# Performance work log

Measured on AMD Instinct MI355X. Metric: run time of the kernel, lower is better.

## Reference

```python
import math
import jax, jax.numpy as jnp
import numpy as np

K_TOP = 8
D_HEAD = 32


def causal_topk_adjacency(x, K):
    # Binary adjacency: for each position t, top-K strictly-causal (j < t)
    # neighbours by dot-product similarity. Rows with < K valid positions
    # (e.g. t=0 has none) get only their valid entries (possibly zero rows).
    B, T, D = x.shape
    sim = jnp.einsum('btd,bsd->bts', x, x) / math.sqrt(D)  # (B,T,T)
    causal = jnp.tril(jnp.ones((T, T), dtype=bool), k=-1)   # j < t
    neg = jnp.finfo(sim.dtype).min
    sim_m = jnp.where(causal[None], sim, neg)
    vals, idx = jax.lax.top_k(sim_m, K)                      # (B,T,K)
    valid = (vals > neg).astype(x.dtype)
    b = jnp.arange(B)[:, None, None]
    t = jnp.arange(T)[None, :, None]
    A = jnp.zeros((B, T, T), x.dtype).at[b, t, idx].max(valid)
    return A


def setup_inputs() -> dict:
    key = jax.random.key(0)
    ks = jax.random.split(key, 3)
    B, T, D = 2, 4096, 1024
    x = jax.random.normal(ks[0], (B, T, D), dtype=jnp.float32)
    W_q = jax.random.normal(ks[1], (D_HEAD, D), dtype=jnp.float32) * (1.0 / math.sqrt(D))
    W_k = jax.random.normal(ks[2], (D_HEAD, D), dtype=jnp.float32) * (1.0 / math.sqrt(D))
    gain = jnp.ones((D,), dtype=jnp.float32)
    bias = jnp.zeros((D,), dtype=jnp.float32)
    log_mix = jnp.zeros((), dtype=jnp.float32)
    log_scale = jnp.zeros((), dtype=jnp.float32)
    return {"x": x, "W_q": W_q, "W_k": W_k, "gain": gain, "bias": bias,
            "log_mix": log_mix, "log_scale": log_scale}


def reference(x, W_q, W_k, gain, bias, log_mix, log_scale):
    B, T, D = x.shape
    mix = jax.nn.sigmoid(log_mix)
    scale = jax.nn.softplus(log_scale) + 0.01

    A = causal_topk_adjacency(x, K_TOP)                      # (B,T,T) binary

    q = jnp.einsum('btd,hd->bth', x, W_q)                    # (B,T,Dh)
    k = jnp.einsum('bsd,hd->bsh', x, W_k)
    score = jnp.einsum('bth,bsh->bts', q, k) / math.sqrt(D_HEAD)
    score = jnp.where(A < 0.5, -1e9, score)

    row_max = jax.lax.stop_gradient(jnp.max(score, axis=-1, keepdims=True))
    score = score - row_max
    attn = jax.nn.softmax(score, axis=-1)
    attn = jnp.nan_to_num(attn, nan=0.0)

    msg = jnp.einsum('bts,bsd->btd', attn, x)
    blended = mix * x + (1.0 - mix) * msg
    delta = jax.nn.gelu(blended * gain + bias, approximate=False) * scale
    return delta
```

## Files before the change

kernel.cpp:

```cpp
#include <hip/hip_runtime.h>
#include <math.h>

#define B 2
#define T 4096
#define D 1024
#define DH 32
#define TNB 32
#define NBLK 528
#define NK 12
#define CPR (32*NK)

typedef __bf16 bf16x8 __attribute__((ext_vector_type(8)));
typedef float f32x4 __attribute__((ext_vector_type(4)));
typedef unsigned u32x4 __attribute__((ext_vector_type(4)));

#define AS1 __attribute__((address_space(1)))
#define AS3 __attribute__((address_space(3)))

__device__ __forceinline__ unsigned mono32(float v) {
    unsigned u = __float_as_uint(v);
    u ^= ((unsigned)((int)u >> 31)) | 0x80000000u;
    return u;
}

__device__ __forceinline__ unsigned dpp_umax_bcast(unsigned v) {
    #define DPPMAX(CTRL) { unsigned t_ = (unsigned)__builtin_amdgcn_update_dpp(0, (int)v, CTRL, 0xF, 0xF, true); v = v > t_ ? v : t_; }
    DPPMAX(0x111) DPPMAX(0x112) DPPMAX(0x114) DPPMAX(0x118)
    DPPMAX(0x142) DPPMAX(0x143)
    #undef DPPMAX
    return (unsigned)__builtin_amdgcn_readlane((int)v, 63);
}
__device__ __forceinline__ float dpp_fsum_bcast(float v) {
    #define DPPADD(CTRL) { int t_ = __builtin_amdgcn_update_dpp(0, __float_as_int(v), CTRL, 0xF, 0xF, true); v += __int_as_float(t_); }
    DPPADD(0x111) DPPADD(0x112) DPPADD(0x114) DPPADD(0x118)
    DPPADD(0x142) DPPADD(0x143)
    #undef DPPADD
    return __int_as_float(__builtin_amdgcn_readlane(__float_as_int(v), 63));
}
__device__ __forceinline__ float dpp_gsum8(float p) {
    { int t_ = __builtin_amdgcn_update_dpp(0, __float_as_int(p), 0x0B1, 0xF, 0xF, true); p += __int_as_float(t_); }
    { int t_ = __builtin_amdgcn_update_dpp(0, __float_as_int(p), 0x04E, 0xF, 0xF, true); p += __int_as_float(t_); }
    { int t_ = __builtin_amdgcn_update_dpp(0, __float_as_int(p), 0x141, 0xF, 0xF, true); p += __int_as_float(t_); }
    return p;
}

__device__ __forceinline__ void merge12(const unsigned* a12, const unsigned* b12,
                                        unsigned* o12) {
    unsigned m16[16];
    #pragma unroll
    for (int i = 0; i < 16; ++i) {
        unsigned aa = (i < NK) ? a12[i] : 0u;
        unsigned bb = (15 - i < NK) ? b12[15 - i] : 0u;
        m16[i] = aa > bb ? aa : bb;
    }
    #pragma unroll
    for (int g = 8; g >= 1; g >>= 1) {
        #pragma unroll
        for (int i = 0; i < 16; ++i) {
            if (!(i & g)) {
                unsigned x0 = m16[i], x1 = m16[i + g];
                m16[i]     = x0 > x1 ? x0 : x1;
                m16[i + g] = x0 > x1 ? x1 : x0;
            }
        }
    }
    #pragma unroll
    for (int i = 0; i < NK; ++i) o12[i] = m16[i];
}

__global__ __launch_bounds__(256) void conv_kernel(const float* __restrict__ x,
        __bf16* __restrict__ xhi, __bf16* __restrict__ xlo)
{
    int i = (blockIdx.x * 256 + threadIdx.x) << 3;
    float4 a = *(const float4*)(x + i);
    float4 c = *(const float4*)(x + i + 4);
    float av[8] = {a.x, a.y, a.z, a.w, c.x, c.y, c.z, c.w};
    __bf16 h[8], l[8];
    #pragma unroll
    for (int j = 0; j < 8; ++j) {
        h[j] = (__bf16)av[j];
        l[j] = (__bf16)(av[j] - (float)h[j]);
    }
    *(float4*)(xhi + i) = *(float4*)h;
    *(float4*)(xlo + i) = *(float4*)l;
}

__global__ void mean_kernel(const float* __restrict__ x, float* __restrict__ meansum)
{
    int gid  = blockIdx.x;
    int b    = gid >> 6;
    int rem  = gid & 63;
    int dblk = rem >> 4;
    int tch  = rem & 15;
    int d = dblk * 256 + threadIdx.x;
    const float* xp = x + (b * T + tch * 256) * D + d;
    float s = 0.f;
    #pragma unroll 8
    for (int it = 0; it < 256; ++it) s += xp[it * D];
    atomicAdd(&meansum[(b << 10) + d], s);
}

__global__ __launch_bounds__(256) void qk_mfma_kernel(
        const __bf16* __restrict__ xhi, const __bf16* __restrict__ xlo,
        const __bf16* __restrict__ Whi, const __bf16* __restrict__ Wlo,
        float* __restrict__ qo, float* __restrict__ ko)
{
    __shared__ __align__(16) __bf16 stg[10240];
    __bf16* sAhi = stg;
    __bf16* sAlo = stg + 2560;
    __bf16* sBhi = stg + 5120;
    __bf16* sBlo = stg + 7680;

    int tid = threadIdx.x;
    int m0 = blockIdx.x << 6;
    int w = tid >> 6, lane = tid & 63;
    int fr = lane & 15, fq = lane >> 4;

    int arow = tid >> 2, aq = tid & 3;
    const __bf16* gAh = xhi + (size_t)(m0 + arow) * D + aq * 8;
    const __bf16* gAl = xlo + (size_t)(m0 + arow) * D + aq * 8;
    const __bf16* gBh = Whi + arow * D + aq * 8;
    const __bf16* gBl = Wlo + arow * D + aq * 8;

    f32x4 acc[4];
    #pragma unroll
    for (int j = 0; j < 4; ++j) acc[j] = (f32x4){0.f, 0.f, 0.f, 0.f};

    float4 a0 = *(const float4*)(gAh);
    float4 a1 = *(const float4*)(gAl);
    float4 b0 = *(const float4*)(gBh);
    float4 b1 = *(const float4*)(gBl);

    int sa = arow * 40 + aq * 8;

    for (int kc = 0; kc < 32; ++kc) {
        __syncthreads();
        *(float4*)(sAhi + sa) = a0;
        *(float4*)(sAlo + sa) = a1;
        *(float4*)(sBhi + sa) = b0;
        *(float4*)(sBlo + sa) = b1;
        __syncthreads();
        if (kc + 1 < 32) {
            int k0 = (kc + 1) << 5;
            a0 = *(const float4*)(gAh + k0);
            a1 = *(const float4*)(gAl + k0);
            b0 = *(const float4*)(gBh + k0);
            b1 = *(const float4*)(gBl + k0);
        }
        int r = (w << 4) + fr;
        bf16x8 fah = *(const bf16x8*)(sAhi + r * 40 + fq * 8);
        bf16x8 fal = *(const bf16x8*)(sAlo + r * 40 + fq * 8);
        bf16x8 fbh[4], fbl[4];
        #pragma unroll
        for (int j = 0; j < 4; ++j) {
            int rb = j * 16 + fr;
            fbh[j] = *(const bf16x8*)(sBhi + rb * 40 + fq * 8);
            fbl[j] = *(const bf16x8*)(sBlo + rb * 40 + fq * 8);
        }
        #pragma unroll
        for (int j = 0; j < 4; ++j) {
            acc[j] = __builtin_amdgcn_mfma_f32_16x16x32_bf16(fah, fbh[j], acc[j], 0, 0, 0);
            acc[j] = __builtin_amdgcn_mfma_f32_16x16x32_bf16(fah, fbl[j], acc[j], 0, 0, 0);
            acc[j] = __builtin_amdgcn_mfma_f32_16x16x32_bf16(fal, fbh[j], acc[j], 0, 0, 0);
        }
    }
    int grow0 = m0 + (w << 4) + (fq << 2);
    #pragma unroll
    for (int j = 0; j < 4; ++j) {
        int gn = j * 16 + fr;
        float* dst = (gn < 32) ? (qo + grow0 * DH + gn)
                               : (ko + grow0 * DH + gn - 32);
        dst[0]      = acc[j][0];
        dst[DH]     = acc[j][1];
        dst[2 * DH] = acc[j][2];
        dst[3 * DH] = acc[j][3];
    }
}

__global__ __launch_bounds__(256, 4) void topk_mfma_kernel(
        const __bf16* __restrict__ xhi, unsigned* __restrict__ pkey)
{
    __shared__ __align__(16) char smem[40960];
    __bf16* stg = (__bf16*)smem;
    float* Sbuf = (float*)smem;

    int tid = threadIdx.x;
    int b = blockIdx.x / NBLK;
    int l = blockIdx.x - b * NBLK;
    int rt = (int)((sqrtf(8.f * l + 1.f) - 1.f) * 0.5f);
    while ((rt + 1) * (rt + 2) / 2 <= l) ++rt;
    while (rt * (rt + 1) / 2 > l) --rt;
    int ct = l - rt * (rt + 1) / 2;
    int r0 = rt << 7, c0 = ct << 7;
    int base = b * T;

    int w = tid >> 6, lane = tid & 63;
    int wr = (w >> 1) << 6, wc = (w & 1) << 6;
    bool active = !(rt == ct && w == 1);
    int fr = lane & 15, fq = lane >> 4;
    int fqs = (fq ^ ((fr >> 1) & 3)) << 3;

    int lrow = lane >> 2;
    int lcq = (((lane & 3) ^ ((lane >> 3) & 3)) << 3);
    const __bf16* gA = xhi + (size_t)(base + r0) * D;
    const __bf16* gB = xhi + (size_t)(base + c0) * D;
    const __bf16* gA0 = gA + (size_t)((w << 4) + lrow) * D + lcq;
    const __bf16* gA1 = gA0 + (size_t)64 * D;
    const __bf16* gB0 = gB + (size_t)((w << 4) + lrow) * D + lcq;
    const __bf16* gB1 = gB0 + (size_t)64 * D;

    f32x4 acc[4][4];
    #pragma unroll
    for (int i = 0; i < 4; ++i)
        #pragma unroll
        for (int j = 0; j < 4; ++j) acc[i][j] = (f32x4){0.f, 0.f, 0.f, 0.f};

#define ISSUE_A(BUFBASE, KO) do { \
    __bf16* bA_ = (BUFBASE); \
    __builtin_amdgcn_global_load_lds((const AS1 unsigned int*)(gA0 + (KO)), \
        (AS3 unsigned int*)(bA_ + (w << 9)), 16, 0, 0); \
    __builtin_amdgcn_global_load_lds((const AS1 unsigned int*)(gA1 + (KO)), \
        (AS3 unsigned int*)(bA_ + 2048 + (w << 9)), 16, 0, 0); \
} while (0)
#define ISSUE_B(BUFBASE, KO) do { \
    __bf16* bB_ = (BUFBASE); \
    __builtin_amdgcn_global_load_lds((const AS1 unsigned int*)(gB0 + (KO)), \
        (AS3 unsigned int*)(bB_ + (w << 9)), 16, 0, 0); \
    __builtin_amdgcn_global_load_lds((const AS1 unsigned int*)(gB1 + (KO)), \
        (AS3 unsigned int*)(bB_ + 2048 + (w << 9)), 16, 0, 0); \
} while (0)

    ISSUE_B(stg + 12288, 0);
    ISSUE_A(stg, 0);
    ISSUE_A(stg + 4096, 32);

    int asel = 0, isel = 2;
    for (int kc = 0; kc < 32; ++kc) {
        if (kc < 31) { asm volatile("s_waitcnt vmcnt(2)" ::: "memory"); }
        else         { asm volatile("s_waitcnt vmcnt(0)" ::: "memory"); }
        __builtin_amdgcn_s_barrier();
        asm volatile("" ::: "memory");
        if (kc + 1 < 32)
            ISSUE_B(stg + 12288 + (((kc + 1) & 1) << 12), (kc + 1) << 5);
        if (kc + 2 < 32) {
            ISSUE_A(stg + (isel << 12), (kc + 2) << 5);
            isel = (isel == 2) ? 0 : isel + 1;
        }
        if (active) {
            const __bf16* cA = stg + (asel << 12);
            const __bf16* cB = stg + 12288 + ((kc & 1) << 12);
            bf16x8 ah[4], bh[4];
            #pragma unroll
            for (int i = 0; i < 4; ++i) {
                int ar = wr + i * 16 + fr;
                ah[i] = *(const bf16x8*)(cA + ar * 32 + fqs);
                int bc = wc + i * 16 + fr;
                bh[i] = *(const bf16x8*)(cB + bc * 32 + fqs);
            }
            #pragma unroll
            for (int i = 0; i < 4; ++i)
                #pragma unroll
                for (int j = 0; j < 4; ++j)
                    acc[i][j] = __builtin_amdgcn_mfma_f32_16x16x32_bf16(ah[i], bh[j], acc[i][j], 0, 0, 0);
        }
        asel = (asel == 2) ? 0 : asel + 1;
    }
#undef ISSUE_A
#undef ISSUE_B

    int cr = fq << 2, cc = fr;
    int q = lane >> 4;
    #pragma unroll
    for (int phase = 0; phase < 2; ++phase) {
        __syncthreads();
        if ((w >> 1) == phase) {
            #pragma unroll
            for (int i = 0; i < 4; ++i)
                #pragma unroll
                for (int j = 0; j < 4; ++j) {
                    float* sp = Sbuf + (i * 16 + cr) * 129 + wc + j * 16 + cc;
                    sp[0]       = acc[i][j][0];
                    sp[129]     = acc[i][j][1];
                    sp[2 * 129] = acc[i][j][2];
                    sp[3 * 129] = acc[i][j][3];
                }
        }
        __syncthreads();
        {
            int sr = (w << 4) + (lane & 15);
            int gt = r0 + (phase << 6) + sr;
            int cmax = gt - c0;
            if (cmax > 128) cmax = 128;
            if (cmax < 0) cmax = 0;
            int h0 = q << 5;
            int hmax = cmax < (h0 + 32) ? cmax : (h0 + 32);
            unsigned key[NK];
            #pragma unroll
            for (int i = 0; i < NK; ++i) key[i] = 0u;
            const float* Srow = Sbuf + sr * 129;
            #pragma unroll
            for (int mb = 0; mb < 4; ++mb) {
                int cb = h0 + (((mb + q) & 3) << 3);
                float v[8];
                #pragma unroll
                for (int j = 0; j < 8; ++j) v[j] = Srow[cb + j];
                #pragma unroll
                for (int j = 0; j < 8; ++j) {
                    int c = cb + j;
                    unsigned u = mono32(v[j]);
                    unsigned tk = (c < hmax) ? ((u & 0xFFFFFF80u) | (unsigned)(127 - c)) : 0u;
                    #pragma unroll
                    for (int i = 0; i < NK; ++i) {
                        unsigned hi = key[i] > tk ? key[i] : tk;
                        unsigned lo = key[i] > tk ? tk : key[i];
                        key[i] = hi; tk = lo;
                    }
                }
            }
            #pragma unroll
            for (int lvl = 0; lvl < 2; ++lvl) {
                int xm = 16 << lvl;
                unsigned o12[NK], m12[NK];
                #pragma unroll
                for (int i = 0; i < NK; ++i) o12[i] = __shfl_xor(key[i], xm);
                merge12(key, o12, m12);
                #pragma unroll
                for (int i = 0; i < NK; ++i) key[i] = m12[i];
            }
            if (q < 3) {
                u32x4 ov;
                #pragma unroll
                for (int j = 0; j < 4; ++j) {
                    unsigned k0 = (q == 0) ? key[j] : (q == 1) ? key[4 + j] : key[8 + j];
                    ov[j] = k0 ? ((k0 & 0xFFFFF000u) | ((k0 & 127u) + (unsigned)(3968 - c0))) : 0u;
                }
                *(u32x4*)(pkey + (size_t)(base + gt) * CPR + ct * NK + (q << 2)) = ov;
            }
        }
    }
}

__global__ __launch_bounds__(256) void select_msg_kernel(const float* __restrict__ x,
        const float* __restrict__ q, const float* __restrict__ k,
        const float* __restrict__ meansum,
        const unsigned* __restrict__ pkey,
        const float* __restrict__ gain, const float* __restrict__ bias,
        const float* __restrict__ plm, const float* __restrict__ pls,
        float* __restrict__ out)
{
    int tid = threadIdx.x;
    int w = tid >> 6, lane = tid & 63;
    int rid = (blockIdx.x << 2) + w;
    int b = rid >> 12, t = rid & (T - 1);
    int ncand = NK * ((t + 127) >> 7);

    unsigned cv[6];
    #pragma unroll
    for (int u = 0; u < 6; ++u) {
        int cid = lane + (u << 6);
        cv[u] = (cid < ncand) ? pkey[(size_t)rid * CPR + cid] : 0u;
    }
    const float* xt = x + (size_t)rid * D;
    float4 xt4[4];
    #pragma unroll
    for (int c = 0; c < 4; ++c)
        xt4[c] = *(const float4*)(xt + (c << 8) + (lane << 2));

    unsigned skey[NK]; int sgid[NK];
    #pragma unroll
    for (int i = 0; i < NK; ++i) {
        unsigned m = cv[0];
        #pragma unroll
        for (int u = 1; u < 6; ++u) m = m > cv[u] ? m : cv[u];
        m = dpp_umax_bcast(m);
        skey[i] = m;
        sgid[i] = 4095 - (int)(m & 4095u);
        #pragma unroll
        for (int u = 0; u < 6; ++u) cv[u] = (cv[u] == m) ? 0u : cv[u];
    }

    float ex[NK];
    #pragma unroll
    for (int batch = 0; batch < 3; ++batch) {
        float4 rv[4][4];
        #pragma unroll
        for (int s = 0; s < 4; ++s) {
            int i = batch * 4 + s;
            int row = (skey[i] != 0u) ? sgid[i] : 0;
            const float* xj = x + (size_t)((b << 12) + row) * D;
            #pragma unroll
            for (int c = 0; c < 4; ++c)
                rv[s][c] = *(const float4*)(xj + (c << 8) + (lane << 2));
        }
        #pragma unroll
        for (int s = 0; s < 4; ++s) {
            float ss = 0.f;
            #pragma unroll
            for (int c = 0; c < 4; ++c)
                ss += xt4[c].x * rv[s][c].x + xt4[c].y * rv[s][c].y
                    + xt4[c].z * rv[s][c].z + xt4[c].w * rv[s][c].w;
            ex[batch * 4 + s] = dpp_fsum_bcast(ss);
        }
    }

    unsigned long long top8[8];
    #pragma unroll
    for (int r = 0; r < 8; ++r) top8[r] = 0ull;
    #pragma unroll
    for (int i = 0; i < NK; ++i) {
        unsigned u = mono32(ex[i]);
        unsigned long long t64 = (skey[i] != 0u)
            ? ((((unsigned long long)u) << 12) | (unsigned long long)(4095 - sgid[i]))
            : 0ull;
        #pragma unroll
        for (int r = 0; r < 8; ++r) {
            unsigned long long hi = (t64 > top8[r]) ? t64 : top8[r];
            unsigned long long lo = (t64 > top8[r]) ? top8[r] : t64;
            top8[r] = hi; t64 = lo;
        }
    }
    bool vld[8]; int bidx[8];
    #pragma unroll
    for (int i = 0; i < 8; ++i) {
        vld[i]  = top8[i] != 0ull;
        bidx[i] = 4095 - (int)(top8[i] & 4095ull);
    }

    int i8 = lane >> 3, e = lane & 7;
    unsigned long long kk = (i8 & 4)
        ? ((i8 & 2) ? ((i8 & 1) ? top8[7] : top8[6]) : ((i8 & 1) ? top8[5] : top8[4]))
        : ((i8 & 2) ? ((i8 & 1) ? top8[3] : top8[2]) : ((i8 & 1) ? top8[1] : top8[0]));
    bool v8 = kk != 0ull;
    int g8 = v8 ? (4095 - (int)(kk & 4095ull)) : 0;
    float4 qv = *(const float4*)(q + (size_t)rid * DH + (e << 2));
    float4 kv = *(const float4*)(k + (size_t)((b << 12) + g8) * DH + (e << 2));
    float p = qv.x * kv.x + qv.y * kv.y + qv.z * kv.z + qv.w * kv.w;
    p = dpp_gsum8(p);
    p *= 0.17677669529663687f;

    float sc[8];
    #pragma unroll
    for (int i = 0; i < 8; ++i)
        sc[i] = __int_as_float(__builtin_amdgcn_readlane(__float_as_int(p), i << 3));

    float m = -INFINITY; int cnt = 0;
    #pragma unroll
    for (int i = 0; i < 8; ++i)
        if (vld[i]) { ++cnt; if (sc[i] > m) m = sc[i]; }

    float wgt[8]; float Z = 0.f; int gsel[8];
    #pragma unroll
    for (int i = 0; i < 8; ++i) {
        wgt[i] = vld[i] ? expf(sc[i] - m) : 0.f;
        Z += wgt[i];
        gsel[i] = vld[i] ? ((b << 12) + bidx[i]) : (b << 12);
    }
    float invZ = (cnt > 0) ? 1.f / Z : 0.f;
    #pragma unroll
    for (int i = 0; i < 8; ++i) wgt[i] *= invZ;

    float mix   = 1.f / (1.f + expf(-plm[0]));
    float scale = log1pf(expf(pls[0])) + 0.01f;
    const float onemix = 1.f - mix;

    float4 msg4[4];
    if (cnt == 0) {
        #pragma unroll
        for (int c = 0; c < 4; ++c) {
            float4 ms = *(const float4*)(meansum + (b << 10) + (c << 8) + (lane << 2));
            msg4[c].x = ms.x * (1.f / (float)T); msg4[c].y = ms.y * (1.f / (float)T);
            msg4[c].z = ms.z * (1.f / (float)T); msg4[c].w = ms.w * (1.f / (float)T);
        }
    } else {
        #pragma unroll
        for (int c = 0; c < 4; ++c) msg4[c] = (float4){0.f, 0.f, 0.f, 0.f};
        #pragma unroll
        for (int g = 0; g < 2; ++g) {
            float4 rv[4][4];
            #pragma unroll
            for (int s = 0; s < 4; ++s) {
                const float* xj = x + (size_t)gsel[g * 4 + s] * D;
                #pragma unroll
                for (int c = 0; c < 4; ++c)
                    rv[s][c] = *(const float4*)(xj + (c << 8) + (lane << 2));
            }
            #pragma unroll
            for (int s = 0; s < 4; ++s) {
                float wi = wgt[g * 4 + s];
                #pragma unroll
                for (int c = 0; c < 4; ++c) {
                    msg4[c].x += wi * rv[s][c].x; msg4[c].y += wi * rv[s][c].y;
                    msg4[c].z += wi * rv[s][c].z; msg4[c].w += wi * rv[s][c].w;
                }
            }
        }
    }
    #pragma unroll
    for (int c = 0; c < 4; ++c) {
        int d0 = (c << 8) + (lane << 2);
        float4 g4 = *(const float4*)(gain + d0);
        float4 b4 = *(const float4*)(bias + d0);
        float4 xv = xt4[c];
        float zi[4] = {
            (mix * xv.x + onemix * msg4[c].x) * g4.x + b4.x,
            (mix * xv.y + onemix * msg4[c].y) * g4.y + b4.y,
            (mix * xv.z + onemix * msg4[c].z) * g4.z + b4.z,
            (mix * xv.w + onemix * msg4[c].w) * g4.w + b4.w };
        float4 o4;
        o4.x = 0.5f * zi[0] * (1.f + erff(zi[0] * 0.70710678118654752f)) * scale;
        o4.y = 0.5f * zi[1] * (1.f + erff(zi[1] * 0.70710678118654752f)) * scale;
        o4.z = 0.5f * zi[2] * (1.f + erff(zi[2] * 0.70710678118654752f)) * scale;
        o4.w = 0.5f * zi[3] * (1.f + erff(zi[3] * 0.70710678118654752f)) * scale;
        *(float4*)(out + (size_t)rid * D + d0) = o4;
    }
}

extern "C" void kernel_launch(void* const* d_in, const int* in_sizes, int n_in,
                              void* d_out, int out_size, void* d_ws, size_t ws_size,
                              hipStream_t stream)
{
    const float* x    = (const float*)d_in[0];
    const float* Wq   = (const float*)d_in[1];
    const float* Wk   = (const float*)d_in[2];
    const float* gain = (const float*)d_in[3];
    const float* bias = (const float*)d_in[4];
    const float* plm  = (const float*)d_in[5];
    const float* pls  = (const float*)d_in[6];
    float* out = (float*)d_out;

    float* ws      = (float*)d_ws;
    float* q       = ws;
    float* k       = ws + 262144;
    float* meansum = ws + 524288;
    unsigned* pkey = (unsigned*)(ws + 526336);
    __bf16* xhi    = (__bf16*)(ws + 3672064);
    __bf16* xlo    = xhi + (size_t)B * T * D;
    __bf16* Whi    = xlo + (size_t)B * T * D;
    __bf16* Wlo    = Whi + 64 * D;

    hipMemsetAsync(meansum, 0, 2048 * sizeof(float), stream);
    conv_kernel<<<B * T * D / 2048, 256, 0, stream>>>(x, xhi, xlo);
    conv_kernel<<<16, 256, 0, stream>>>(Wq, Whi, Wlo);
    conv_kernel<<<16, 256, 0, stream>>>(Wk, Whi + 32 * D, Wlo + 32 * D);
    mean_kernel<<<128, 256, 0, stream>>>(x, meansum);
    qk_mfma_kernel<<<B * T / 64, 256, 0, stream>>>(xhi, xlo, Whi, Wlo, q, k);
    topk_mfma_kernel<<<B * NBLK, 256, 0, stream>>>(xhi, pkey);
    select_msg_kernel<<<B * T / 4, 256, 0, stream>>>(x, q, k, meansum, pkey,
                                                     gain, bias, plm, pls, out);
}
```

Before: 262.6 us.

## Fuse prep kernels and merge QK projection with top-k launch

The x and W bf16 conversion kernels and the column-mean kernel become one prep launch. The mean now writes per-chunk partial sums, so the memset and atomics go away and select_msg reduces the 16 partials itself. The QK projection blocks and the top-k similarity blocks share a single launch, and the top-k blocks get an index swizzle to spread tile shapes across batches. This removes several launches and lets the small QK GEMM overlap with top-k, but it adds branch divergence and pushes qk blocks to the occupancy limit of the top-k kernel.

```diff
diff --git a/kernel.cpp b/kernel.cpp
--- a/kernel.cpp
+++ b/kernel.cpp
@@ -68,12 +68,11 @@
     for (int i = 0; i < NK; ++i) o12[i] = m16[i];
 }
 
-__global__ __launch_bounds__(256) void conv_kernel(const float* __restrict__ x,
-        __bf16* __restrict__ xhi, __bf16* __restrict__ xlo)
+__device__ __forceinline__ void conv_body(const float* __restrict__ src,
+        __bf16* __restrict__ dhi, __bf16* __restrict__ dlo, int i)
 {
-    int i = (blockIdx.x * 256 + threadIdx.x) << 3;
-    float4 a = *(const float4*)(x + i);
-    float4 c = *(const float4*)(x + i + 4);
+    float4 a = *(const float4*)(src + i);
+    float4 c = *(const float4*)(src + i + 4);
     float av[8] = {a.x, a.y, a.z, a.w, c.x, c.y, c.z, c.w};
     __bf16 h[8], l[8];
     #pragma unroll
@@ -81,112 +80,127 @@
         h[j] = (__bf16)av[j];
         l[j] = (__bf16)(av[j] - (float)h[j]);
     }
-    *(float4*)(xhi + i) = *(float4*)h;
-    *(float4*)(xlo + i) = *(float4*)l;
-}
-
-__global__ void mean_kernel(const float* __restrict__ x, float* __restrict__ meansum)
+    *(float4*)(dhi + i) = *(float4*)h;
+    *(float4*)(dlo + i) = *(float4*)l;
+}
+
+__global__ __launch_bounds__(256) void prep_kernel(const float* __restrict__ x,
+        const float* __restrict__ Wq, const float* __restrict__ Wk,
+        __bf16* __restrict__ xhi, __bf16* __restrict__ xlo,
+        __bf16* __restrict__ Whi, __bf16* __restrict__ Wlo,
+        float* __restrict__ meansum2)
 {
-    int gid  = blockIdx.x;
-    int b    = gid >> 6;
-    int rem  = gid & 63;
-    int dblk = rem >> 4;
-    int tch  = rem & 15;
-    int d = dblk * 256 + threadIdx.x;
-    const float* xp = x + (b * T + tch * 256) * D + d;
-    float s = 0.f;
-    #pragma unroll 8
-    for (int it = 0; it < 256; ++it) s += xp[it * D];
-    atomicAdd(&meansum[(b << 10) + d], s);
-}
-
-__global__ __launch_bounds__(256) void qk_mfma_kernel(
+    int g = blockIdx.x;
+    if (g < 4096) {
+        conv_body(x, xhi, xlo, (g * 256 + threadIdx.x) << 3);
+    } else if (g < 4128) {
+        int gw = g - 4096;
+        const float* src = (gw < 16) ? Wq : Wk;
+        __bf16* dhi = Whi + ((gw < 16) ? 0 : 32 * D);
+        __bf16* dlo = Wlo + ((gw < 16) ? 0 : 32 * D);
+        conv_body(src, dhi, dlo, ((gw & 15) * 256 + threadIdx.x) << 3);
+    } else {
+        int gm = g - 4128;
+        int b = gm >> 6;
+        int rem = gm & 63;
+        int dblk = rem >> 4;
+        int tch = rem & 15;
+        int d = dblk * 256 + threadIdx.x;
+        const float* xp = x + (b * T + tch * 256) * D + d;
+        float s = 0.f;
+        #pragma unroll 8
+        for (int it = 0; it < 256; ++it) s += xp[it * D];
+        meansum2[(((b << 4) + tch) << 10) + d] = s;
+    }
+}
+
+__global__ __launch_bounds__(256, 4) void qk_topk_kernel(
         const __bf16* __restrict__ xhi, const __bf16* __restrict__ xlo,
         const __bf16* __restrict__ Whi, const __bf16* __restrict__ Wlo,
-        float* __restrict__ qo, float* __restrict__ ko)
+        float* __restrict__ qo, float* __restrict__ ko,
+        unsigned* __restrict__ pkey)
 {
-    __shared__ __align__(16) __bf16 stg[10240];
-    __bf16* sAhi = stg;
-    __bf16* sAlo = stg + 2560;
-    __bf16* sBhi = stg + 5120;
-    __bf16* sBlo = stg + 7680;
-
+    __shared__ __align__(16) char smem[40960];
     int tid = threadIdx.x;
-    int m0 = blockIdx.x << 6;
     int w = tid >> 6, lane = tid & 63;
     int fr = lane & 15, fq = lane >> 4;
 
-    int arow = tid >> 2, aq = tid & 3;
-    const __bf16* gAh = xhi + (size_t)(m0 + arow) * D + aq * 8;
-    const __bf16* gAl = xlo + (size_t)(m0 + arow) * D + aq * 8;
-    const __bf16* gBh = Whi + arow * D + aq * 8;
-    const __bf16* gBl = Wlo + arow * D + aq * 8;
-
-    f32x4 acc[4];
-    #pragma unroll
-    for (int j = 0; j < 4; ++j) acc[j] = (f32x4){0.f, 0.f, 0.f, 0.f};
-
-    float4 a0 = *(const float4*)(gAh);
-    float4 a1 = *(const float4*)(gAl);
-    float4 b0 = *(const float4*)(gBh);
-    float4 b1 = *(const float4*)(gBl);
-
-    int sa = arow * 40 + aq * 8;
-
-    for (int kc = 0; kc < 32; ++kc) {
-        __syncthreads();
-        *(float4*)(sAhi + sa) = a0;
-        *(float4*)(sAlo + sa) = a1;
-        *(float4*)(sBhi + sa) = b0;
-        *(float4*)(sBlo + sa) = b1;
-        __syncthreads();
-        if (kc + 1 < 32) {
-            int k0 = (kc + 1) << 5;
-            a0 = *(const float4*)(gAh + k0);
-            a1 = *(const float4*)(gAl + k0);
-            b0 = *(const float4*)(gBh + k0);
-            b1 = *(const float4*)(gBl + k0);
-        }
-        int r = (w << 4) + fr;
-        bf16x8 fah = *(const bf16x8*)(sAhi + r * 40 + fq * 8);
-        bf16x8 fal = *(const bf16x8*)(sAlo + r * 40 + fq * 8);
-        bf16x8 fbh[4], fbl[4];
+    if (blockIdx.x < 128) {
+        __bf16* sAhi = (__bf16*)smem;
+        __bf16* sAlo = sAhi + 2560;
+        __bf16* sBhi = sAhi + 5120;
+        __bf16* sBlo = sAhi + 7680;
+
+        int m0 = blockIdx.x << 6;
+        int arow = tid >> 2, aq = tid & 3;
+        const __bf16* gAh = xhi + (size_t)(m0 + arow) * D + aq * 8;
+        const __bf16* gAl = xlo + (size_t)(m0 + arow) * D + aq * 8;
+        const __bf16* gBh = Whi + arow * D + aq * 8;
+        const __bf16* gBl = Wlo + arow * D + aq * 8;
+
+        f32x4 acc[4];
+        #pragma unroll
+        for (int j = 0; j < 4; ++j) acc[j] = (f32x4){0.f, 0.f, 0.f, 0.f};
+
+        float4 a0 = *(const float4*)(gAh);
+        float4 a1 = *(const float4*)(gAl);
+        float4 b0 = *(const float4*)(gBh);
+        float4 b1 = *(const float4*)(gBl);
+
+        int sa = arow * 40 + aq * 8;
+
+        for (int kc = 0; kc < 32; ++kc) {
+            __syncthreads();
+            *(float4*)(sAhi + sa) = a0;
+            *(float4*)(sAlo + sa) = a1;
+            *(float4*)(sBhi + sa) = b0;
+            *(float4*)(sBlo + sa) = b1;
+            __syncthreads();
+            if (kc + 1 < 32) {
+                int k0 = (kc + 1) << 5;
+                a0 = *(const float4*)(gAh + k0);
+                a1 = *(const float4*)(gAl + k0);
+                b0 = *(const float4*)(gBh + k0);
+                b1 = *(const float4*)(gBl + k0);
+            }
+            int r = (w << 4) + fr;
+            bf16x8 fah = *(const bf16x8*)(sAhi + r * 40 + fq * 8);
+            bf16x8 fal = *(const bf16x8*)(sAlo + r * 40 + fq * 8);
+            bf16x8 fbh[4], fbl[4];
+            #pragma unroll
+            for (int j = 0; j < 4; ++j) {
+                int rb = j * 16 + fr;
+                fbh[j] = *(const bf16x8*)(sBhi + rb * 40 + fq * 8);
+                fbl[j] = *(const bf16x8*)(sBlo + rb * 40 + fq * 8);
+            }
+            #pragma unroll
+            for (int j = 0; j < 4; ++j) {
+                acc[j] = __builtin_amdgcn_mfma_f32_16x16x32_bf16(fah, fbh[j], acc[j], 0, 0, 0);
+                acc[j] = __builtin_amdgcn_mfma_f32_16x16x32_bf16(fah, fbl[j], acc[j], 0, 0, 0);
+                acc[j] = __builtin_amdgcn_mfma_f32_16x16x32_bf16(fal, fbh[j], acc[j], 0, 0, 0);
+            }
+        }
+        int grow0 = m0 + (w << 4) + (fq << 2);
         #pragma unroll
         for (int j = 0; j < 4; ++j) {
-            int rb = j * 16 + fr;
-            fbh[j] = *(const bf16x8*)(sBhi + rb * 40 + fq * 8);
-            fbl[j] = *(const bf16x8*)(sBlo + rb * 40 + fq * 8);
-        }
-        #pragma unroll
-        for (int j = 0; j < 4; ++j) {
-            acc[j] = __builtin_amdgcn_mfma_f32_16x16x32_bf16(fah, fbh[j], acc[j], 0, 0, 0);
-            acc[j] = __builtin_amdgcn_mfma_f32_16x16x32_bf16(fah, fbl[j], acc[j], 0, 0, 0);
-            acc[j] = __builtin_amdgcn_mfma_f32_16x16x32_bf16(fal, fbh[j], acc[j], 0, 0, 0);
-        }
-    }
-    int grow0 = m0 + (w << 4) + (fq << 2);
-    #pragma unroll
-    for (int j = 0; j < 4; ++j) {
-        int gn = j * 16 + fr;
-        float* dst = (gn < 32) ? (qo + grow0 * DH + gn)
-                               : (ko + grow0 * DH + gn - 32);
-        dst[0]      = acc[j][0];
-        dst[DH]     = acc[j][1];
-        dst[2 * DH] = acc[j][2];
-        dst[3 * DH] = acc[j][3];
-    }
-}
-
-__global__ __launch_bounds__(256, 4) void topk_mfma_kernel(
-        const __bf16* __restrict__ xhi, unsigned* __restrict__ pkey)
-{
-    __shared__ __align__(16) char smem[40960];
+            int gn = j * 16 + fr;
+            float* dst = (gn < 32) ? (qo + grow0 * DH + gn)
+                                   : (ko + grow0 * DH + gn - 32);
+            dst[0]      = acc[j][0];
+            dst[DH]     = acc[j][1];
+            dst[2 * DH] = acc[j][2];
+            dst[3 * DH] = acc[j][3];
+        }
+        return;
+    }
+
     __bf16* stg = (__bf16*)smem;
     float* Sbuf = (float*)smem;
 
-    int tid = threadIdx.x;
-    int b = blockIdx.x / NBLK;
-    int l = blockIdx.x - b * NBLK;
+    int p = blockIdx.x - 128;
+    int swz = (p & 7) * 132 + (p >> 3);
+    int b = swz / NBLK;
+    int l = swz - b * NBLK;
     int rt = (int)((sqrtf(8.f * l + 1.f) - 1.f) * 0.5f);
     while ((rt + 1) * (rt + 2) / 2 <= l) ++rt;
     while (rt * (rt + 1) / 2 > l) --rt;
@@ -194,10 +208,8 @@
     int r0 = rt << 7, c0 = ct << 7;
     int base = b * T;
 
-    int w = tid >> 6, lane = tid & 63;
     int wr = (w >> 1) << 6, wc = (w & 1) << 6;
     bool active = !(rt == ct && w == 1);
-    int fr = lane & 15, fq = lane >> 4;
     int fqs = (fq ^ ((fr >> 1) & 3)) << 3;
 
     int lrow = lane >> 2;
@@ -342,7 +354,7 @@
 
 __global__ __launch_bounds__(256) void select_msg_kernel(const float* __restrict__ x,
         const float* __restrict__ q, const float* __restrict__ k,
-        const float* __restrict__ meansum,
+        const float* __restrict__ meansum2,
         const unsigned* __restrict__ pkey,
         const float* __restrict__ gain, const float* __restrict__ bias,
         const float* __restrict__ plm, const float* __restrict__ pls,
@@ -467,9 +479,15 @@
     if (cnt == 0) {
         #pragma unroll
         for (int c = 0; c < 4; ++c) {
-            float4 ms = *(const float4*)(meansum + (b << 10) + (c << 8) + (lane << 2));
-            msg4[c].x = ms.x * (1.f / (float)T); msg4[c].y = ms.y * (1.f / (float)T);
-            msg4[c].z = ms.z * (1.f / (float)T); msg4[c].w = ms.w * (1.f / (float)T);
+            int d0 = (c << 8) + (lane << 2);
+            float4 a4 = (float4){0.f, 0.f, 0.f, 0.f};
+            #pragma unroll
+            for (int tch = 0; tch < 16; ++tch) {
+                float4 ms = *(const float4*)(meansum2 + (((b << 4) + tch) << 10) + d0);
+                a4.x += ms.x; a4.y += ms.y; a4.z += ms.z; a4.w += ms.w;
+            }
+            msg4[c].x = a4.x * (1.f / (float)T); msg4[c].y = a4.y * (1.f / (float)T);
+            msg4[c].z = a4.z * (1.f / (float)T); msg4[c].w = a4.w * (1.f / (float)T);
         }
     } else {
         #pragma unroll
@@ -528,23 +546,18 @@
     const float* pls  = (const float*)d_in[6];
     float* out = (float*)d_out;
 
-    float* ws      = (float*)d_ws;
-    float* q       = ws;
-    float* k       = ws + 262144;
-    float* meansum = ws + 524288;
-    unsigned* pkey = (unsigned*)(ws + 526336);
-    __bf16* xhi    = (__bf16*)(ws + 3672064);
-    __bf16* xlo    = xhi + (size_t)B * T * D;
-    __bf16* Whi    = xlo + (size_t)B * T * D;
-    __bf16* Wlo    = Whi + 64 * D;
-
-    hipMemsetAsync(meansum, 0, 2048 * sizeof(float), stream);
-    conv_kernel<<<B * T * D / 2048, 256, 0, stream>>>(x, xhi, xlo);
-    conv_kernel<<<16, 256, 0, stream>>>(Wq, Whi, Wlo);
-    conv_kernel<<<16, 256, 0, stream>>>(Wk, Whi + 32 * D, Wlo + 32 * D);
-    mean_kernel<<<128, 256, 0, stream>>>(x, meansum);
-    qk_mfma_kernel<<<B * T / 64, 256, 0, stream>>>(xhi, xlo, Whi, Wlo, q, k);
-    topk_mfma_kernel<<<B * NBLK, 256, 0, stream>>>(xhi, pkey);
-    select_msg_kernel<<<B * T / 4, 256, 0, stream>>>(x, q, k, meansum, pkey,
+    float* ws       = (float*)d_ws;
+    float* q        = ws;
+    float* k        = ws + 262144;
+    float* meansum2 = ws + 524288;
+    unsigned* pkey  = (unsigned*)(ws + 557056);
+    __bf16* xhi     = (__bf16*)(ws + 3702784);
+    __bf16* xlo     = xhi + (size_t)B * T * D;
+    __bf16* Whi     = xlo + (size_t)B * T * D;
+    __bf16* Wlo     = Whi + 64 * D;
+
+    prep_kernel<<<4256, 256, 0, stream>>>(x, Wq, Wk, xhi, xlo, Whi, Wlo, meansum2);
+    qk_topk_kernel<<<128 + B * NBLK, 256, 0, stream>>>(xhi, xlo, Whi, Wlo, q, k, pkey);
+    select_msg_kernel<<<B * T / 4, 256, 0, stream>>>(x, q, k, meansum2, pkey,
                                                      gain, bias, plm, pls, out);
 }
```

Result: faster. 233.4 us (-11.1%).
